# Performance work log

Measured on AMD Instinct MI355X. Metric: run time of the kernel, lower is better.

Reference implementation:

```python
import jax, jax.numpy as jnp
import numpy as np

B = 32          # number of graphs
N_PER = 1000    # num_nodes per graph (CDSQN.num_nodes)
TOTAL = B * N_PER
E = 512000      # edges (avg degree 16)
F_IN = 128      # node_feat_dim
HID = 128       # hidden_dim (= GNN embedding_dim)
D = 64          # dsf_hidden_dim
NH = 3          # num_heads
EPS = 1e-6


def setup_inputs() -> dict:
    key = jax.random.key(0)
    ks = jax.random.split(key, 12)
    x = jax.random.normal(ks[0], (TOTAL, F_IN), jnp.float32)
    edge_index = jax.random.randint(ks[1], (2, E), 0, TOTAL, dtype=jnp.int64)
    batch_index = jnp.repeat(jnp.arange(B, dtype=jnp.int64), N_PER)
    actions = (jax.random.uniform(ks[2], (B, N_PER)) < 0.1).astype(jnp.float32)

    def lin(k, fan_in, fan_out):
        s = 1.0 / np.sqrt(fan_in)
        return jax.random.uniform(k, (fan_in, fan_out), jnp.float32, -s, s)

    Wc1 = lin(ks[3], F_IN, HID); bc1 = jnp.zeros((HID,), jnp.float32)
    Wc2 = lin(ks[4], HID, HID);  bc2 = jnp.zeros((HID,), jnp.float32)
    Wc3 = lin(ks[5], HID, HID);  bc3 = jnp.zeros((HID,), jnp.float32)
    Wg1 = lin(ks[6], HID, NH * N_PER * D); bg1 = jnp.full((NH * N_PER * D,), 0.1, jnp.float32)
    Wg2 = lin(ks[7], HID, NH * D * D);     bg2 = jnp.full((NH * D * D,), 0.1, jnp.float32)
    Wg3 = lin(ks[8], HID, NH * D);         bg3 = jnp.full((NH * D,), 0.1, jnp.float32)
    return dict(x=x, edge_index=edge_index, batch_index=batch_index, actions=actions,
                Wc1=Wc1, bc1=bc1, Wc2=Wc2, bc2=bc2, Wc3=Wc3, bc3=bc3,
                Wg1=Wg1, bg1=bg1, Wg2=Wg2, bg2=bg2, Wg3=Wg3, bg3=bg3)


def _gcn(h, W, b, src, dst, norm):
    # PyG GCNConv: h' = D^-1/2 (A+I) D^-1/2 (h W) + b ; src/dst include self loops
    h = h @ W
    msgs = h[src] * norm[:, None]            # [E+TOTAL, out]
    return jax.ops.segment_sum(msgs, dst, num_segments=TOTAL) + b


def reference(x, edge_index, batch_index, actions,
              Wc1, bc1, Wc2, bc2, Wc3, bc3,
              Wg1, bg1, Wg2, bg2, Wg3, bg3):
    loops = jnp.arange(TOTAL, dtype=edge_index.dtype)
    src = jnp.concatenate([edge_index[0], loops])
    dst = jnp.concatenate([edge_index[1], loops])
    deg = jax.ops.segment_sum(jnp.ones(src.shape[0], x.dtype), dst, num_segments=TOTAL)
    dinv = jnp.where(deg > 0, jax.lax.rsqrt(deg), 0.0)
    norm = dinv[src] * dinv[dst]

    h = jax.nn.relu(_gcn(x, Wc1, bc1, src, dst, norm))
    h = jax.nn.relu(_gcn(h, Wc2, bc2, src, dst, norm))
    h = _gcn(h, Wc3, bc3, src, dst, norm)

    # global_mean_pool
    cnt = jax.ops.segment_sum(jnp.ones(TOTAL, x.dtype), batch_index, num_segments=B)
    h_g = jax.ops.segment_sum(h, batch_index, num_segments=B) / cnt[:, None]  # [B, HID]

    # hypernetwork weights
    w1 = jax.nn.softplus((h_g @ Wg1 + bg1).reshape(B, NH, N_PER, D))
    w2 = jax.nn.softplus((h_g @ Wg2 + bg2).reshape(B, NH, D, D))
    w3 = jax.nn.softplus((h_g @ Wg3 + bg3).reshape(B, NH, D))

    # compute_q (2D actions branch)
    h1 = jnp.einsum('bn,bhnd->bhd', actions, w1)
    h1 = jnp.sqrt(jnp.clip(h1, 0.0) + EPS)           # SafeSqrt
    h2 = jnp.einsum('bhd,bhde->bhe', h1, w2)
    h2 = jnp.log1p(jnp.clip(h2, 0.0))                # SafeLog: log(1+clamp(x,0))
    out_heads = jnp.einsum('bhd,bhd->bh', h2, w3)    # [B, NH]
    return jnp.min(out_heads, axis=-1)               # [B]
```

## Files before the change

### kernel.cpp

```cpp
#include <hip/hip_runtime.h>
#include <hip/hip_bf16.h>
#include <math.h>

#define NB 32
#define N_PER 1000
#define TOTALN 32000
#define NE 512000
#define HID 128
#define Dh 64
#define NH 3
#define EPSV 1e-6f
#define PCH 25
#define W1CH 500

typedef __attribute__((ext_vector_type(8))) short bf16x8;
typedef __attribute__((ext_vector_type(4))) float f32x4;

__device__ __forceinline__ float softplusf(float x) {
    return fmaxf(x, 0.0f) + log1pf(expf(-fabsf(x)));
}
__device__ __forceinline__ unsigned short f2b(float f) {
    __hip_bfloat16 h = __float2bfloat16(f);
    return __builtin_bit_cast(unsigned short, h);
}
__device__ __forceinline__ float b2f(unsigned short u) {
    unsigned int x = ((unsigned int)u) << 16;
    return __builtin_bit_cast(float, x);
}

__global__ __launch_bounds__(256) void k_init(float* deg, float* h1pre) {
    int i = blockIdx.x * 256 + threadIdx.x;
    if (i < TOTALN) deg[i] = 1.0f;
    if (i < 96 * 64) h1pre[i] = 0.f;
}

__global__ __launch_bounds__(256) void k_deg(const int* __restrict__ ei, float* deg) {
    int e = blockIdx.x * 256 + threadIdx.x;
    if (e < NE) atomicAdd(&deg[ei[NE + e]], 1.0f);
}

__global__ __launch_bounds__(256) void k_scan1(float* __restrict__ deg,
                                               int* __restrict__ rowptr,
                                               int* __restrict__ bsum) {
    __shared__ int sh[256];
    int t = threadIdx.x;
    int i = blockIdx.x * 256 + t;
    float dv = deg[i];
    int v = (int)dv - 1;
    deg[i] = rsqrtf(dv);
    sh[t] = v;
    __syncthreads();
    for (int off = 1; off < 256; off <<= 1) {
        int add = (t >= off) ? sh[t - off] : 0;
        __syncthreads();
        sh[t] += add;
        __syncthreads();
    }
    rowptr[i] = sh[t] - v;
    if (t == 255) bsum[blockIdx.x] = sh[255];
}

__global__ __launch_bounds__(256) void k_scan2(int* __restrict__ rowptr,
                                               const int* __restrict__ bsum,
                                               int* __restrict__ cursor) {
    __shared__ int sh[128];
    __shared__ int spre;
    int t = threadIdx.x, bid = blockIdx.x;
    if (t < 125) sh[t] = bsum[t];
    __syncthreads();
    if (t == 0) {
        int run = 0;
        for (int j = 0; j < bid; ++j) run += sh[j];
        spre = run;
    }
    __syncthreads();
    int i = bid * 256 + t;
    int v = rowptr[i] + spre;
    rowptr[i] = v;
    cursor[i] = v;
    if (i == 0) rowptr[TOTALN] = NE;
}

__global__ __launch_bounds__(256) void k_fill(const int* __restrict__ ei,
                                              const float* __restrict__ dinv,
                                              int* __restrict__ cursor,
                                              int* __restrict__ csr_src,
                                              float* __restrict__ csr_w) {
    int e = blockIdx.x * 256 + threadIdx.x;
    if (e < NE) {
        int s = ei[e], d = ei[NE + e];
        int pos = atomicAdd(&cursor[d], 1);
        csr_src[pos] = s;
        csr_w[pos] = dinv[s] * dinv[d];
    }
}

__global__ __launch_bounds__(256) void k_wcvt3(const float* __restrict__ W1,
                                               const float* __restrict__ W2,
                                               const float* __restrict__ W3,
                                               unsigned short* __restrict__ Wt) {
    int i = blockIdx.x * 256 + threadIdx.x;
    int w = i >> 14, j = i & 16383;
    const float* W = (w == 0) ? W1 : (w == 1) ? W2 : W3;
    int k = j >> 7, c = j & 127;
    Wt[w * 16384 + c * 128 + k] = f2b(W[j]);
}

template<int INF32>
__global__ __launch_bounds__(256) void k_mm(const void* __restrict__ Xv,
                                            const unsigned short* __restrict__ Wt,
                                            unsigned short* __restrict__ Y) {
    int tid = threadIdx.x;
    int wv = tid >> 6, l = tid & 63;
    int row0 = blockIdx.x * 64 + wv * 16;
    int r = l & 15, kc = l >> 4;
    bf16x8 a[4];
    if (INF32) {
        const float* X = (const float*)Xv;
#pragma unroll
        for (int ks = 0; ks < 4; ++ks) {
            const float* p = X + (long)(row0 + r) * 128 + ks * 32 + kc * 8;
            float4 f0 = *(const float4*)p;
            float4 f1 = *(const float4*)(p + 4);
            bf16x8 t;
            t[0] = (short)f2b(f0.x); t[1] = (short)f2b(f0.y);
            t[2] = (short)f2b(f0.z); t[3] = (short)f2b(f0.w);
            t[4] = (short)f2b(f1.x); t[5] = (short)f2b(f1.y);
            t[6] = (short)f2b(f1.z); t[7] = (short)f2b(f1.w);
            a[ks] = t;
        }
    } else {
        const unsigned short* X = (const unsigned short*)Xv;
#pragma unroll
        for (int ks = 0; ks < 4; ++ks)
            a[ks] = *(const bf16x8*)(X + (long)(row0 + r) * 128 + ks * 32 + kc * 8);
    }
    f32x4 acc[8];
#pragma unroll
    for (int nt = 0; nt < 8; ++nt) acc[nt] = (f32x4){0.f, 0.f, 0.f, 0.f};
#pragma unroll
    for (int ks = 0; ks < 4; ++ks) {
#pragma unroll
        for (int nt = 0; nt < 8; ++nt) {
            bf16x8 b = *(const bf16x8*)(Wt + (nt * 16 + r) * 128 + ks * 32 + kc * 8);
            acc[nt] = __builtin_amdgcn_mfma_f32_16x16x32_bf16(a[ks], b, acc[nt], 0, 0, 0);
        }
    }
#pragma unroll
    for (int nt = 0; nt < 8; ++nt)
#pragma unroll
        for (int j = 0; j < 4; ++j)
            Y[(long)(row0 + kc * 4 + j) * 128 + nt * 16 + r] = f2b(acc[nt][j]);
}

template<int MODE>
__global__ __launch_bounds__(256) void k_gather(const unsigned short* __restrict__ feat,
                                                unsigned short* __restrict__ out,
                                                const int* __restrict__ rowptr,
                                                const int* __restrict__ csr_src,
                                                const float* __restrict__ csr_w,
                                                const float* __restrict__ dinv,
                                                const float* __restrict__ bias) {
    int wid = threadIdx.x >> 6, lane = threadIdx.x & 63;
    int v = blockIdx.x * 4 + wid;
    const unsigned int* f2 = (const unsigned int*)feat;
    float dv = dinv[v];
    unsigned int sv = f2[v * 64 + lane];
    float acc0 = b2f((unsigned short)(sv & 0xffff)) * dv * dv;
    float acc1 = b2f((unsigned short)(sv >> 16)) * dv * dv;
    int e = rowptr[v], e1 = rowptr[v + 1];
    for (; e + 4 <= e1; e += 4) {
        int s0 = csr_src[e], s1 = csr_src[e + 1], s2 = csr_src[e + 2], s3 = csr_src[e + 3];
        float w0 = csr_w[e], w1 = csr_w[e + 1], w2 = csr_w[e + 2], w3 = csr_w[e + 3];
        unsigned int u0 = f2[s0 * 64 + lane];
        unsigned int u1 = f2[s1 * 64 + lane];
        unsigned int u2 = f2[s2 * 64 + lane];
        unsigned int u3 = f2[s3 * 64 + lane];
        acc0 += b2f((unsigned short)(u0 & 0xffff)) * w0 + b2f((unsigned short)(u1 & 0xffff)) * w1
              + b2f((unsigned short)(u2 & 0xffff)) * w2 + b2f((unsigned short)(u3 & 0xffff)) * w3;
        acc1 += b2f((unsigned short)(u0 >> 16)) * w0 + b2f((unsigned short)(u1 >> 16)) * w1
              + b2f((unsigned short)(u2 >> 16)) * w2 + b2f((unsigned short)(u3 >> 16)) * w3;
    }
    for (; e < e1; ++e) {
        int s = csr_src[e];
        float w = csr_w[e];
        unsigned int u = f2[s * 64 + lane];
        acc0 += b2f((unsigned short)(u & 0xffff)) * w;
        acc1 += b2f((unsigned short)(u >> 16)) * w;
    }
    if (MODE == 0) {
        int c = lane * 2;
        acc0 = fmaxf(acc0 + bias[c], 0.f);
        acc1 = fmaxf(acc1 + bias[c + 1], 0.f);
    }
    ((unsigned int*)out)[v * 64 + lane] =
        (unsigned int)f2b(acc0) | ((unsigned int)f2b(acc1) << 16);
}

__global__ __launch_bounds__(256) void k_pool1(const unsigned short* __restrict__ A,
                                               float* __restrict__ pp) {
    __shared__ float sh[256];
    int b = blockIdx.x / PCH, ch = blockIdx.x % PCH;
    int c = threadIdx.x & 127, half = threadIdx.x >> 7;
    float acc = 0.f;
    int n0 = ch * 40;
#pragma unroll 4
    for (int j = half; j < 40; j += 2)
        acc += b2f(A[(long)(b * N_PER + n0 + j) * 128 + c]);
    sh[threadIdx.x] = acc;
    __syncthreads();
    if (threadIdx.x < 128)
        pp[blockIdx.x * 128 + c] = sh[c] + sh[128 + c];
}

__global__ __launch_bounds__(256) void k_pool2(const float* __restrict__ pp,
                                               const float* __restrict__ bias,
                                               float* __restrict__ hg,
                                               unsigned short* __restrict__ hgB) {
    int i = blockIdx.x * 256 + threadIdx.x;
    if (i >= NB * 128) return;
    int b = i >> 7, c = i & 127;
    float s = 0.f;
#pragma unroll
    for (int ch = 0; ch < PCH; ++ch)
        s += pp[(b * PCH + ch) * 128 + c];
    float v = s * (1.0f / N_PER) + bias[c];
    hg[i] = v;
    hgB[i] = f2b(v);
}

__global__ __launch_bounds__(256) void k_w1(const unsigned short* __restrict__ hgB,
                                            const float* __restrict__ Wg1,
                                            const float* __restrict__ bg1,
                                            const float* __restrict__ actions,
                                            float* __restrict__ p1) {
    __shared__ unsigned short wt[2][64][136];
    int h = blockIdx.x / W1CH, chunk = blockIdx.x % W1CH;
    int tid = threadIdx.x;
    int wv = tid >> 6, l = tid & 63;
    int r = l & 15, kc = l >> 4;
    const long KS = (long)NH * N_PER * Dh;
    int n0 = chunk * 2;
    long colbase2 = (long)h * (N_PER * Dh) + (long)n0 * Dh;
    bf16x8 a[2][4];
#pragma unroll
    for (int mt = 0; mt < 2; ++mt)
#pragma unroll
        for (int ks = 0; ks < 4; ++ks)
            a[mt][ks] = *(const bf16x8*)(hgB + (mt * 16 + r) * 128 + ks * 32 + kc * 8);
    int kq = tid >> 5;
    int j = (tid & 31) * 4;
    int ns = j >> 6, ds = j & 63;
#pragma unroll 4
    for (int it = 0; it < 16; ++it) {
        int k = it * 8 + kq;
        float4 v = *(const float4*)(Wg1 + (long)k * KS + colbase2 + j);
        wt[ns][ds][k]     = f2b(v.x);
        wt[ns][ds + 1][k] = f2b(v.y);
        wt[ns][ds + 2][k] = f2b(v.z);
        wt[ns][ds + 3][k] = f2b(v.w);
    }
    __syncthreads();
#pragma unroll
    for (int nn = 0; nn < 2; ++nn) {
        int n = n0 + nn;
        f32x4 acc0 = (f32x4){0.f, 0.f, 0.f, 0.f};
        f32x4 acc1 = (f32x4){0.f, 0.f, 0.f, 0.f};
#pragma unroll
        for (int ks = 0; ks < 4; ++ks) {
            bf16x8 bb = *(const bf16x8*)&wt[nn][wv * 16 + r][ks * 32 + kc * 8];
            acc0 = __builtin_amdgcn_mfma_f32_16x16x32_bf16(a[0][ks], bb, acc0, 0, 0, 0);
            acc1 = __builtin_amdgcn_mfma_f32_16x16x32_bf16(a[1][ks], bb, acc1, 0, 0, 0);
        }
        float bgv = bg1[colbase2 + nn * 64 + wv * 16 + r];
        float* po = p1 + ((long)h * N_PER + n) * 2048;
#pragma unroll
        for (int jj = 0; jj < 4; ++jj) {
            int b0 = kc * 4 + jj;
            int b1 = 16 + kc * 4 + jj;
            po[b0 * 64 + wv * 16 + r] = softplusf(acc0[jj] + bgv) * actions[b0 * N_PER + n];
            po[b1 * 64 + wv * 16 + r] = softplusf(acc1[jj] + bgv) * actions[b1 * N_PER + n];
        }
    }
}

__global__ __launch_bounds__(256) void k_red1a(const float* __restrict__ p1,
                                               float* __restrict__ h1pre) {
    __shared__ float sh[4][64];
    int bh = blockIdx.x >> 3, seg = blockIdx.x & 7;
    int b = bh / 3, h = bh % 3;
    int part = threadIdx.x >> 6, d = threadIdx.x & 63;
    const float* base = p1 + (long)h * N_PER * 2048 + b * 64 + d;
    float s = 0.f;
    for (int n = seg * 125 + part; n < seg * 125 + 125; n += 4)
        s += base[(long)n * 2048];
    if (part) sh[part][d] = s;
    __syncthreads();
    if (part == 0)
        atomicAdd(&h1pre[bh * 64 + d], s + sh[1][d] + sh[2][d] + sh[3][d]);
}

__global__ __launch_bounds__(256) void k_w2(const float* __restrict__ hg,
                                            const float* __restrict__ Wg2,
                                            const float* __restrict__ bg2,
                                            const float* __restrict__ h1pre,
                                            float* __restrict__ p2) {
    __shared__ float hgs[32][128];
    __shared__ float wt[128][64];
    __shared__ float h1s[32];
    int hd = blockIdx.x;
    int tid = threadIdx.x;
    for (int i = 0; i < 16; ++i) {
        int idx = tid + i * 256;
        hgs[idx >> 7][idx & 127] = hg[idx];
    }
    long base = (long)hd * 64;
    for (int i = 0; i < 32; ++i) {
        int idx = tid + i * 256;
        wt[idx >> 6][idx & 63] = Wg2[(long)(idx >> 6) * (NH * Dh * Dh) + base + (idx & 63)];
    }
    int h = hd >> 6, d = hd & 63;
    if (tid < 32)
        h1s[tid] = sqrtf(fmaxf(h1pre[(tid * 3 + h) * 64 + d], 0.f) + EPSV);
    __syncthreads();
    int e = tid & 63, bq = tid >> 6;
    float bgv = bg2[base + e];
    float dot[8];
#pragma unroll
    for (int bi = 0; bi < 8; ++bi) dot[bi] = 0.f;
    for (int k = 0; k < 128; ++k) {
        float w = wt[k][e];
#pragma unroll
        for (int bi = 0; bi < 8; ++bi)
            dot[bi] += hgs[bq * 8 + bi][k] * w;
    }
    float* po = p2 + (long)hd * (32 * 64);
#pragma unroll
    for (int bi = 0; bi < 8; ++bi) {
        int b = bq * 8 + bi;
        po[b * 64 + e] = softplusf(dot[bi] + bgv) * h1s[b];
    }
}

__global__ __launch_bounds__(192) void k_out(const float* __restrict__ hg,
                                             const float* __restrict__ Wg3,
                                             const float* __restrict__ bg3,
                                             const float* __restrict__ p2,
                                             float* __restrict__ out) {
    __shared__ float hgb[128];
    __shared__ float hres[NH];
    int b = blockIdx.x, tid = threadIdx.x;
    if (tid < 128) hgb[tid] = hg[b * 128 + tid];
    __syncthreads();
    int h = tid / 64, e = tid & 63;
    int c = h * 64 + e;
    float s = 0.f;
#pragma unroll 8
    for (int d = 0; d < 64; ++d)
        s += p2[(long)(h * 64 + d) * 2048 + b * 64 + e];
    float h2v = log1pf(fmaxf(s, 0.f));
    float dot = 0.f;
    for (int k = 0; k < 128; ++k)
        dot += hgb[k] * Wg3[k * (NH * Dh) + c];
    float v = softplusf(dot + bg3[c]) * h2v;
    for (int off = 32; off; off >>= 1)
        v += __shfl_down(v, off, 64);
    if (e == 0) hres[h] = v;
    __syncthreads();
    if (tid == 0) out[b] = fminf(fminf(hres[0], hres[1]), hres[2]);
}

extern "C" void kernel_launch(void* const* d_in, const int* in_sizes, int n_in,
                              void* d_out, int out_size, void* d_ws, size_t ws_size,
                              hipStream_t stream) {
    const float* x   = (const float*)d_in[0];
    const int*   ei  = (const int*)d_in[1];
    const float* act = (const float*)d_in[3];
    const float* Wc1 = (const float*)d_in[4];
    const float* bc1 = (const float*)d_in[5];
    const float* Wc2 = (const float*)d_in[6];
    const float* bc2 = (const float*)d_in[7];
    const float* Wc3 = (const float*)d_in[8];
    const float* bc3 = (const float*)d_in[9];
    const float* Wg1 = (const float*)d_in[10];
    const float* bg1 = (const float*)d_in[11];
    const float* Wg2 = (const float*)d_in[12];
    const float* bg2 = (const float*)d_in[13];
    const float* Wg3 = (const float*)d_in[14];
    const float* bg3 = (const float*)d_in[15];
    float* out = (float*)d_out;

    float* ws   = (float*)d_ws;
    float* dinv = ws;
    float* bufA = dinv + TOTALN;
    float* bufB = bufA + (long)TOTALN * 128;
    float* hg   = bufB + (long)TOTALN * 128;
    float* h1pre = hg + 32 * 128;
    float* csr_w = h1pre + 96 * 64;
    float* pp   = csr_w + NE;
    unsigned short* hgB = (unsigned short*)(pp + NB * PCH * 128);
    int* rowptr = (int*)(hgB + 4096);
    int* cursor = rowptr + TOTALN + 4;
    int* bsum   = cursor + TOTALN;
    int* csr_src= bsum + 128;
    unsigned short* Wt = (unsigned short*)(csr_src + NE);
    unsigned short* fA = (unsigned short*)bufA;
    unsigned short* fB = (unsigned short*)bufB;
    float* p1   = bufA;
    float* p2   = bufA + (long)3 * N_PER * 2048;

    k_init<<<(TOTALN + 255) / 256, 256, 0, stream>>>(dinv, h1pre);
    k_deg<<<NE / 256, 256, 0, stream>>>(ei, dinv);
    k_scan1<<<125, 256, 0, stream>>>(dinv, rowptr, bsum);
    k_scan2<<<125, 256, 0, stream>>>(rowptr, bsum, cursor);
    k_fill<<<NE / 256, 256, 0, stream>>>(ei, dinv, cursor, csr_src, csr_w);
    k_wcvt3<<<192, 256, 0, stream>>>(Wc1, Wc2, Wc3, Wt);

    k_mm<1><<<500, 256, 0, stream>>>(x, Wt, fB);
    k_gather<0><<<TOTALN / 4, 256, 0, stream>>>(fB, fA, rowptr, csr_src, csr_w, dinv, bc1);
    k_mm<0><<<500, 256, 0, stream>>>(fA, Wt + 16384, fB);
    k_gather<0><<<TOTALN / 4, 256, 0, stream>>>(fB, fA, rowptr, csr_src, csr_w, dinv, bc2);
    k_mm<0><<<500, 256, 0, stream>>>(fA, Wt + 32768, fB);
    k_gather<1><<<TOTALN / 4, 256, 0, stream>>>(fB, fA, rowptr, csr_src, csr_w, dinv, nullptr);
    k_pool1<<<NB * PCH, 256, 0, stream>>>(fA, pp);
    k_pool2<<<(NB * 128 + 255) / 256, 256, 0, stream>>>(pp, bc3, hg, hgB);

    k_w1<<<NH * W1CH, 256, 0, stream>>>(hgB, Wg1, bg1, act, p1);
    k_red1a<<<96 * 8, 256, 0, stream>>>(p1, h1pre);
    k_w2<<<NH * Dh, 256, 0, stream>>>(hg, Wg2, bg2, h1pre, p2);
    k_out<<<NB, 192, 0, stream>>>(hg, Wg3, bg3, p2, out);
}
```

Measured before the change: 267.1 us.

## Split GCN gather edges across four lane groups with 16-byte loads

The neighbour-gather kernel now splits each wavefront into four 16-lane groups. Each group handles every fourth edge and loads 8 bf16 features per lane with uint4 loads, where before every lane read 2 features from every edge. Partial sums are combined with cross-lane shuffles and only the first group writes the result. This raises memory-level parallelism per node for the gather step. The cost is extra shuffle reductions and more accumulator registers.

```diff
diff --git a/kernel.cpp b/kernel.cpp
--- a/kernel.cpp
+++ b/kernel.cpp
@@ -26,6 +26,16 @@
 __device__ __forceinline__ float b2f(unsigned short u) {
     unsigned int x = ((unsigned int)u) << 16;
     return __builtin_bit_cast(float, x);
+}
+__device__ __forceinline__ void acc8(float* a, uint4 u, float w) {
+    a[0] += b2f((unsigned short)(u.x & 0xffff)) * w;
+    a[1] += b2f((unsigned short)(u.x >> 16)) * w;
+    a[2] += b2f((unsigned short)(u.y & 0xffff)) * w;
+    a[3] += b2f((unsigned short)(u.y >> 16)) * w;
+    a[4] += b2f((unsigned short)(u.z & 0xffff)) * w;
+    a[5] += b2f((unsigned short)(u.z >> 16)) * w;
+    a[6] += b2f((unsigned short)(u.w & 0xffff)) * w;
+    a[7] += b2f((unsigned short)(u.w >> 16)) * w;
 }
 
 __global__ __launch_bounds__(256) void k_init(float* deg, float* h1pre) {
@@ -162,39 +172,52 @@
                                                 const float* __restrict__ dinv,
                                                 const float* __restrict__ bias) {
     int wid = threadIdx.x >> 6, lane = threadIdx.x & 63;
+    int grp = lane >> 4, li = lane & 15;
     int v = blockIdx.x * 4 + wid;
-    const unsigned int* f2 = (const unsigned int*)feat;
+    const uint4* f16 = (const uint4*)feat;
     float dv = dinv[v];
-    unsigned int sv = f2[v * 64 + lane];
-    float acc0 = b2f((unsigned short)(sv & 0xffff)) * dv * dv;
-    float acc1 = b2f((unsigned short)(sv >> 16)) * dv * dv;
-    int e = rowptr[v], e1 = rowptr[v + 1];
-    for (; e + 4 <= e1; e += 4) {
-        int s0 = csr_src[e], s1 = csr_src[e + 1], s2 = csr_src[e + 2], s3 = csr_src[e + 3];
-        float w0 = csr_w[e], w1 = csr_w[e + 1], w2 = csr_w[e + 2], w3 = csr_w[e + 3];
-        unsigned int u0 = f2[s0 * 64 + lane];
-        unsigned int u1 = f2[s1 * 64 + lane];
-        unsigned int u2 = f2[s2 * 64 + lane];
-        unsigned int u3 = f2[s3 * 64 + lane];
-        acc0 += b2f((unsigned short)(u0 & 0xffff)) * w0 + b2f((unsigned short)(u1 & 0xffff)) * w1
-              + b2f((unsigned short)(u2 & 0xffff)) * w2 + b2f((unsigned short)(u3 & 0xffff)) * w3;
-        acc1 += b2f((unsigned short)(u0 >> 16)) * w0 + b2f((unsigned short)(u1 >> 16)) * w1
-              + b2f((unsigned short)(u2 >> 16)) * w2 + b2f((unsigned short)(u3 >> 16)) * w3;
-    }
-    for (; e < e1; ++e) {
-        int s = csr_src[e];
-        float w = csr_w[e];
-        unsigned int u = f2[s * 64 + lane];
-        acc0 += b2f((unsigned short)(u & 0xffff)) * w;
-        acc1 += b2f((unsigned short)(u >> 16)) * w;
-    }
-    if (MODE == 0) {
-        int c = lane * 2;
-        acc0 = fmaxf(acc0 + bias[c], 0.f);
-        acc1 = fmaxf(acc1 + bias[c + 1], 0.f);
-    }
-    ((unsigned int*)out)[v * 64 + lane] =
-        (unsigned int)f2b(acc0) | ((unsigned int)f2b(acc1) << 16);
+    uint4 sv = f16[v * 16 + li];
+    float a[8] = {0.f, 0.f, 0.f, 0.f, 0.f, 0.f, 0.f, 0.f};
+    if (grp == 0) acc8(a, sv, dv * dv);
+    int e1 = rowptr[v + 1];
+    int i = rowptr[v] + grp;
+    for (; i + 12 < e1; i += 16) {
+        int s0 = csr_src[i], s1 = csr_src[i + 4], s2 = csr_src[i + 8], s3 = csr_src[i + 12];
+        float w0 = csr_w[i], w1 = csr_w[i + 4], w2 = csr_w[i + 8], w3 = csr_w[i + 12];
+        uint4 u0 = f16[s0 * 16 + li];
+        uint4 u1 = f16[s1 * 16 + li];
+        uint4 u2 = f16[s2 * 16 + li];
+        uint4 u3 = f16[s3 * 16 + li];
+        acc8(a, u0, w0);
+        acc8(a, u1, w1);
+        acc8(a, u2, w2);
+        acc8(a, u3, w3);
+    }
+    for (; i < e1; i += 4) {
+        int s = csr_src[i];
+        float w = csr_w[i];
+        uint4 u = f16[s * 16 + li];
+        acc8(a, u, w);
+    }
+#pragma unroll
+    for (int c = 0; c < 8; ++c) {
+        a[c] += __shfl_xor(a[c], 16, 64);
+        a[c] += __shfl_xor(a[c], 32, 64);
+    }
+    if (grp == 0) {
+        if (MODE == 0) {
+            int c0 = li * 8;
+#pragma unroll
+            for (int c = 0; c < 8; ++c)
+                a[c] = fmaxf(a[c] + bias[c0 + c], 0.f);
+        }
+        uint4 o;
+        o.x = (unsigned int)f2b(a[0]) | ((unsigned int)f2b(a[1]) << 16);
+        o.y = (unsigned int)f2b(a[2]) | ((unsigned int)f2b(a[3]) << 16);
+        o.z = (unsigned int)f2b(a[4]) | ((unsigned int)f2b(a[5]) << 16);
+        o.w = (unsigned int)f2b(a[6]) | ((unsigned int)f2b(a[7]) << 16);
+        ((uint4*)out)[v * 16 + li] = o;
+    }
 }
 
 __global__ __launch_bounds__(256) void k_pool1(const unsigned short* __restrict__ A,
```

Result: faster. 256.4 us (-4.0%).
